# Kernel optimization log

Hardware: AMD Instinct MI355X
Metric: run time of the kernel (lower is better)

The kernel has to match this reference:

```python
import jax, jax.numpy as jnp
import numpy as np

# ---- Cl(3,0,1) projective geometric algebra tables (GATr basis ordering) ----
_BASIS = [(), (0,), (1,), (2,), (3,),
          (0, 1), (0, 2), (0, 3), (1, 2), (1, 3), (2, 3),
          (0, 1, 2), (0, 1, 3), (0, 2, 3), (1, 2, 3), (0, 1, 2, 3)]
_IDX = {b: i for i, b in enumerate(_BASIS)}
_METRIC = (0.0, 1.0, 1.0, 1.0)  # e0^2 = 0, e1^2 = e2^2 = e3^2 = 1


def _blade_product(a, b):
    arr = list(a) + list(b)
    sign = 1.0
    for i in range(len(arr)):
        for j in range(len(arr) - 1):
            if arr[j] > arr[j + 1]:
                arr[j], arr[j + 1] = arr[j + 1], arr[j]
                sign = -sign
    out, i = [], 0
    while i < len(arr):
        if i + 1 < len(arr) and arr[i] == arr[i + 1]:
            sign *= _METRIC[arr[i]]
            i += 2
        else:
            out.append(arr[i])
            i += 1
    return sign, tuple(out)


def _build_cayley():
    c = np.zeros((16, 16, 16), np.float32)
    for i, a in enumerate(_BASIS):
        for j, b in enumerate(_BASIS):
            s, blade = _blade_product(a, b)
            if s != 0.0:
                c[i, j, _IDX[blade]] += s
    return c

_CAYLEY = _build_cayley()                      # (16,16,16) geometric-product table
_DUAL_FLIP = np.arange(15, -1, -1)             # index reversal permutation
_DUAL_SIGNS = np.array([_blade_product(_BASIS[15 - j], _BASIS[j])[0] for j in range(16)], np.float32)


def _embed_point(p):
    # GATr-style PGA point embedding into trivector components: mv dim 16
    mv = jnp.zeros(p.shape[:-1] + (16,), p.dtype)
    mv = mv.at[..., 14].set(1.0)          # e123 (homogeneous coord)
    mv = mv.at[..., 13].set(p[..., 0])    # e023 <- x
    mv = mv.at[..., 12].set(-p[..., 1])   # e013 <- -y
    mv = mv.at[..., 11].set(p[..., 2])    # e012 <- z
    return mv


def _nn_gather(query, points):
    # brute-force K=1 NN: for each query point return its nearest neighbor in `points`
    # squared distances (B,N,M) via ||q||^2 + ||p||^2 - 2 q.p
    d = (jnp.sum(query * query, -1)[..., :, None]
         + jnp.sum(points * points, -1)[..., None, :]
         - 2.0 * jnp.einsum('bnd,bmd->bnm', query, points))
    idx = jnp.argmin(d, axis=-1)  # (B,N) int32
    return jnp.take_along_axis(points, idx[..., None], axis=1)  # (B,N,3)


def _geometric_product_loss(pred, tgt):
    cayley = jnp.asarray(_CAYLEY, pred.dtype)
    gp = jnp.einsum('ijk,...i,...j->...k', cayley, pred, tgt)  # (B,N,16)
    diff = pred - tgt
    dual = jnp.asarray(_DUAL_SIGNS, diff.dtype) * diff[..., _DUAL_FLIP]
    loss = jnp.mean(jnp.linalg.norm(gp, axis=-1) + jnp.linalg.norm(dual, axis=-1))
    # normalize to [0,1] with min_loss=1.0, max_loss=3.0
    return jnp.clip((loss - 1.0) / 2.0, 0.0, 1.0)


def setup_inputs() -> dict:
    key = jax.random.key(0)
    k1, k2 = jax.random.split(key)
    B, N = 2, 8192
    return {
        'source_points': jax.random.normal(k1, (B, N, 3), jnp.float32),
        'target_points': jax.random.normal(k2, (B, N, 3), jnp.float32),
    }


def reference(source_points, target_points):
    # source -> nearest target, target -> nearest source
    new_target_points = _nn_gather(source_points, target_points)  # (B,N,3)
    new_source_points = _nn_gather(target_points, source_points)  # (B,N,3)

    mv_source = _embed_point(source_points)
    mv_target = _embed_point(target_points)
    mv_new_source = _embed_point(new_source_points)
    mv_new_target = _embed_point(new_target_points)

    gp_loss_t2s = _geometric_product_loss(mv_source, mv_new_target)
    gp_loss_s2t = _geometric_product_loss(mv_new_source, mv_target)
    return 0.5 * (gp_loss_t2s + gp_loss_s2t)
```

## Files before the change

### kernel.cpp

```cpp
#include <hip/hip_runtime.h>


typedef short short8 __attribute__((ext_vector_type(8)));
typedef float f32x16 __attribute__((ext_vector_type(16)));

#define PPB      1024
#define PS       8
#define LDS_HALF 576
#define LDS_TILE 1152


__device__ __forceinline__ unsigned short bf16h(float f) {
    unsigned u = __float_as_uint(f);
    return (unsigned short)((u + 0x7fffu + ((u >> 16) & 1u)) >> 16);
}
__device__ __forceinline__ float bf16v(unsigned short h) {
    return __uint_as_float((unsigned)h << 16);
}

__global__ __launch_bounds__(256, 4)
void fused_kernel(const float* __restrict__ src, const float* __restrict__ tgt,
                  unsigned* __restrict__ chunkCnt, unsigned* __restrict__ finalCnt,
                  unsigned* __restrict__ accP, unsigned* __restrict__ d2min,
                  float* __restrict__ out, int N) {
    __shared__ __align__(16) unsigned char Alds[32 * LDS_TILE];

    const int t   = threadIdx.x;
    const int l   = t & 63, w = t >> 6;
    const int nqc = N >> 8;
    const int bpt = nqc * PS;
    const int task = blockIdx.x / bpt;
    const int rem  = blockIdx.x % bpt;
    const int qc = rem / PS, pc = rem % PS;

    const int pcloud = task ^ 2;
    const float* pRaw = (pcloud < 2 ? src : tgt)
                        + (size_t)3 * ((size_t)(pcloud & 1) * N + (size_t)pc * PPB);
    #pragma unroll
    for (int k = 0; k < 4; ++k) {
        const int j = t + k * 256;
        const float x = pRaw[3*j], y = pRaw[3*j+1], z = pRaw[3*j+2];
        const float pp = x*x + y*y + z*z;
        unsigned short A16[16];
        const float p3[3] = {x, y, z};
        #pragma unroll
        for (int d = 0; d < 3; ++d) {
            const float m2 = -2.0f * p3[d];
            const unsigned short th = bf16h(m2);
            A16[d] = th; A16[4+d] = th; A16[8+d] = bf16h(m2 - bf16v(th));
        }
        const unsigned short pph = bf16h(pp);
        A16[3] = pph; A16[7] = bf16h(pp - bf16v(pph)); A16[11] = 0;
        A16[12] = A16[13] = A16[14] = A16[15] = 0;
        const int tile = j >> 5, r = j & 31;
        unsigned char* base = Alds + tile * LDS_TILE + r * 16 + (r >> 3) * 16;
        *(short8*)(base)            = *(const short8*)(A16);
        *(short8*)(base + LDS_HALF) = *(const short8*)(A16 + 8);
    }

    const int col = l & 31, h = l >> 5;
    const float* qRaw = (task < 2 ? src : tgt)
                        + (size_t)3 * (size_t)((task & 1) * N);
    const int qloc = qc * 256 + w * 64 + col;
    float qa[3], qb[3];
    #pragma unroll
    for (int d = 0; d < 3; ++d) {
        qa[d] = qRaw[3*qloc + d];
        qb[d] = qRaw[3*(qloc+32) + d];
    }
    const float qqa = qa[0]*qa[0] + qa[1]*qa[1] + qa[2]*qa[2];
    const float qqb = qb[0]*qb[0] + qb[1]*qb[1] + qb[2]*qb[2];

    unsigned short B0[8], B1[8];
    #pragma unroll
    for (int d = 0; d < 3; ++d) {
        const unsigned short ha = bf16h(qa[d]);
        const unsigned short hb = bf16h(qb[d]);
        B0[d] = ha; B1[d] = hb;
        B0[4+d] = (h == 0) ? bf16h(qa[d] - bf16v(ha)) : (unsigned short)0;
        B1[4+d] = (h == 0) ? bf16h(qb[d] - bf16v(hb)) : (unsigned short)0;
    }
    B0[3] = B0[7] = (h == 0) ? (unsigned short)0x3F80 : (unsigned short)0;
    B1[3] = B1[7] = B0[3];
    const short8 b0 = *(const short8*)B0;
    const short8 b1 = *(const short8*)B1;

    __syncthreads();

    const int lbase = h * LDS_HALF + col * 16 + (col >> 3) * 16;
    float best0 = 3.4e38f, best1 = 3.4e38f;
    const f32x16 zero = {};
    #pragma unroll 4
    for (int i = 0; i < 32; ++i) {
        const short8 a = *(const short8*)(Alds + i * LDS_TILE + lbase);
        f32x16 d0 = __builtin_amdgcn_mfma_f32_32x32x16_bf16(a, b0, zero, 0, 0, 0);
        f32x16 d1 = __builtin_amdgcn_mfma_f32_32x32x16_bf16(a, b1, zero, 0, 0, 0);
        best0 = fminf(fminf(d0[0],  d0[1]),  best0);
        best0 = fminf(fminf(d0[2],  d0[3]),  best0);
        best0 = fminf(fminf(d0[4],  d0[5]),  best0);
        best0 = fminf(fminf(d0[6],  d0[7]),  best0);
        best0 = fminf(fminf(d0[8],  d0[9]),  best0);
        best0 = fminf(fminf(d0[10], d0[11]), best0);
        best0 = fminf(fminf(d0[12], d0[13]), best0);
        best0 = fminf(fminf(d0[14], d0[15]), best0);
        best1 = fminf(fminf(d1[0],  d1[1]),  best1);
        best1 = fminf(fminf(d1[2],  d1[3]),  best1);
        best1 = fminf(fminf(d1[4],  d1[5]),  best1);
        best1 = fminf(fminf(d1[6],  d1[7]),  best1);
        best1 = fminf(fminf(d1[8],  d1[9]),  best1);
        best1 = fminf(fminf(d1[10], d1[11]), best1);
        best1 = fminf(fminf(d1[12], d1[13]), best1);
        best1 = fminf(fminf(d1[14], d1[15]), best1);
    }

    best0 = fminf(best0, __shfl_xor(best0, 32));
    best1 = fminf(best1, __shfl_xor(best1, 32));
    const int qbase = task * N + qc * 256;
    if (l < 32) {
        const int q0 = qbase + w * 64 + l;
        unsigned o0 = atomicMin(&d2min[q0],
                                __float_as_uint(fmaxf(best0 + qqa, 0.0f)));
        unsigned o1 = atomicMin(&d2min[q0 + 32],
                                __float_as_uint(fmaxf(best1 + qqb, 0.0f)));
        asm volatile("" :: "v"(o0), "v"(o1));
    }

    __shared__ int lastChunk;
    __syncthreads();
    if (t == 0)
        lastChunk = (atomicAdd(&chunkCnt[task * nqc + qc], 1u)
                     == 0x7f7f7f7fu + (unsigned)PS - 1u);
    __syncthreads();
    if (!lastChunk) return;

    const float d2 = __uint_as_float(atomicOr(&d2min[qbase + t], 0u));
    double fv = (double)(sqrtf(1.0f + d2) + sqrtf(d2));
    #pragma unroll
    for (int o = 32; o > 0; o >>= 1) fv += __shfl_down(fv, o);
    __shared__ double wsum[4];
    __shared__ int lastFinal;
    if (l == 0) wsum[w] = fv;
    __syncthreads();
    if (t == 0) {
        const float csum = (float)(wsum[0] + wsum[1] + wsum[2] + wsum[3]);
        unsigned oldA = atomicExch(&accP[task * nqc + qc], __float_as_uint(csum));
        asm volatile("" :: "v"(oldA));
        lastFinal = (atomicAdd(finalCnt, 1u)
                     == 0x7f7f7f7fu + (unsigned)(4 * nqc) - 1u);
    }
    __syncthreads();
    if (!lastFinal) return;

    __shared__ float pvals[128];
    const int ncid = 4 * nqc;
    if (t < ncid) pvals[t] = __uint_as_float(atomicOr(&accP[t], 0u));
    __syncthreads();
    if (t == 0) {
        double s0 = 0.0, s1 = 0.0;
        for (int i = 0; i < ncid / 2; ++i)        s0 += (double)pvals[i];
        for (int i = ncid / 2; i < ncid; ++i)     s1 += (double)pvals[i];
        const double inv = 1.0 / (double)(2 * N);
        double l0 = (s0 * inv - 1.0) * 0.5;
        double l1 = (s1 * inv - 1.0) * 0.5;
        l0 = l0 < 0.0 ? 0.0 : (l0 > 1.0 ? 1.0 : l0);
        l1 = l1 < 0.0 ? 0.0 : (l1 > 1.0 ? 1.0 : l1);
        out[0] = (float)(0.5 * (l0 + l1));
    }
}

extern "C" void kernel_launch(void* const* d_in, const int* in_sizes, int n_in,
                              void* d_out, int out_size, void* d_ws, size_t ws_size,
                              hipStream_t stream) {
    const float* src = (const float*)d_in[0];
    const float* tgt = (const float*)d_in[1];
    float* out = (float*)d_out;

    const int twoN = in_sizes[0] / 3;
    const int N    = twoN / 2;
    const int QT   = 4 * N;

    unsigned* chunkCnt = (unsigned*)d_ws;
    unsigned* finalCnt = (unsigned*)((char*)d_ws + 512);
    unsigned* accP     = (unsigned*)((char*)d_ws + 1024);
    unsigned* d2min    = (unsigned*)((char*)d_ws + 2048);

    hipMemsetAsync(d_ws, 0x7f, 2048 + (size_t)QT * sizeof(unsigned), stream);

    const int blocks = 4 * (N >> 8) * PS;
    fused_kernel<<<blocks, 256, 0, stream>>>(src, tgt, chunkCnt, finalCnt,
                                             accP, d2min, out, N);
}
```

Baseline: 24.78 us.

## Give each block full point range with double-buffered LDS, drop atomicMin merge

The work split changes from query-chunk × point-chunk blocks (1024 blocks, 256 queries each) to 256 blocks of 128 queries that each scan all 8192 points. Point chunks are staged through a double-buffered LDS pair, so the next chunk is prepared while the current one is processed. This removes the global atomicMin buffer, the per-chunk counters and the large memset, and the final reduction becomes a shuffle-based double-precision sum. The trade-off is fewer blocks, which lowers parallelism and occupancy across the GPU's CUs, and each block now runs a much longer serial loop.

```diff
diff --git a/kernel.cpp b/kernel.cpp
--- a/kernel.cpp
+++ b/kernel.cpp
@@ -4,10 +4,10 @@
 typedef short short8 __attribute__((ext_vector_type(8)));
 typedef float f32x16 __attribute__((ext_vector_type(16)));
 
-#define PPB      1024
-#define PS       8
 #define LDS_HALF 576
 #define LDS_TILE 1152
+#define CHUNK    1024
+#define NCHUNK   8
 
 
 __device__ __forceinline__ unsigned short bf16h(float f) {
@@ -18,147 +18,151 @@
     return __uint_as_float((unsigned)h << 16);
 }
 
-__global__ __launch_bounds__(256, 4)
+__global__ __launch_bounds__(256)
 void fused_kernel(const float* __restrict__ src, const float* __restrict__ tgt,
-                  unsigned* __restrict__ chunkCnt, unsigned* __restrict__ finalCnt,
-                  unsigned* __restrict__ accP, unsigned* __restrict__ d2min,
+                  unsigned* __restrict__ finalCnt,
+                  unsigned long long* __restrict__ accP,
                   float* __restrict__ out, int N) {
-    __shared__ __align__(16) unsigned char Alds[32 * LDS_TILE];
+    __shared__ __align__(16) unsigned char Alds[2][32 * LDS_TILE];
 
     const int t   = threadIdx.x;
     const int l   = t & 63, w = t >> 6;
-    const int nqc = N >> 8;
-    const int bpt = nqc * PS;
-    const int task = blockIdx.x / bpt;
-    const int rem  = blockIdx.x % bpt;
-    const int qc = rem / PS, pc = rem % PS;
-
-    const int pcloud = task ^ 2;
-    const float* pRaw = (pcloud < 2 ? src : tgt)
-                        + (size_t)3 * ((size_t)(pcloud & 1) * N + (size_t)pc * PPB);
-    #pragma unroll
-    for (int k = 0; k < 4; ++k) {
-        const int j = t + k * 256;
-        const float x = pRaw[3*j], y = pRaw[3*j+1], z = pRaw[3*j+2];
-        const float pp = x*x + y*y + z*z;
-        unsigned short A16[16];
-        const float p3[3] = {x, y, z};
-        #pragma unroll
-        for (int d = 0; d < 3; ++d) {
-            const float m2 = -2.0f * p3[d];
-            const unsigned short th = bf16h(m2);
-            A16[d] = th; A16[4+d] = th; A16[8+d] = bf16h(m2 - bf16v(th));
-        }
-        const unsigned short pph = bf16h(pp);
-        A16[3] = pph; A16[7] = bf16h(pp - bf16v(pph)); A16[11] = 0;
-        A16[12] = A16[13] = A16[14] = A16[15] = 0;
-        const int tile = j >> 5, r = j & 31;
-        unsigned char* base = Alds + tile * LDS_TILE + r * 16 + (r >> 3) * 16;
-        *(short8*)(base)            = *(const short8*)(A16);
-        *(short8*)(base + LDS_HALF) = *(const short8*)(A16 + 8);
-    }
+    const int nqc = N >> 7;
+    const int task = blockIdx.x / nqc;
+    const int qc   = blockIdx.x % nqc;
 
     const int col = l & 31, h = l >> 5;
     const float* qRaw = (task < 2 ? src : tgt)
                         + (size_t)3 * (size_t)((task & 1) * N);
-    const int qloc = qc * 256 + w * 64 + col;
-    float qa[3], qb[3];
+    const int qloc = qc * 128 + w * 32 + col;
+    float q3[3];
+    #pragma unroll
+    for (int d = 0; d < 3; ++d) q3[d] = qRaw[3 * qloc + d];
+    const float qq = q3[0]*q3[0] + q3[1]*q3[1] + q3[2]*q3[2];
+
+    unsigned short B8[8];
     #pragma unroll
     for (int d = 0; d < 3; ++d) {
-        qa[d] = qRaw[3*qloc + d];
-        qb[d] = qRaw[3*(qloc+32) + d];
+        const unsigned short qh = bf16h(q3[d]);
+        B8[d] = qh;
+        B8[4 + d] = (h == 0) ? bf16h(q3[d] - bf16v(qh)) : (unsigned short)0;
     }
-    const float qqa = qa[0]*qa[0] + qa[1]*qa[1] + qa[2]*qa[2];
-    const float qqb = qb[0]*qb[0] + qb[1]*qb[1] + qb[2]*qb[2];
+    B8[3] = B8[7] = (h == 0) ? (unsigned short)0x3F80 : (unsigned short)0;
+    const short8 b = *(const short8*)B8;
 
-    unsigned short B0[8], B1[8];
-    #pragma unroll
-    for (int d = 0; d < 3; ++d) {
-        const unsigned short ha = bf16h(qa[d]);
-        const unsigned short hb = bf16h(qb[d]);
-        B0[d] = ha; B1[d] = hb;
-        B0[4+d] = (h == 0) ? bf16h(qa[d] - bf16v(ha)) : (unsigned short)0;
-        B1[4+d] = (h == 0) ? bf16h(qb[d] - bf16v(hb)) : (unsigned short)0;
+    const int pcloud = task ^ 2;
+    const float* pBase = (pcloud < 2 ? src : tgt)
+                         + (size_t)3 * (size_t)((pcloud & 1) * N);
+
+    {
+        const float* pRaw = pBase;
+        #pragma unroll
+        for (int k = 0; k < 4; ++k) {
+            const int j = t + k * 256;
+            const float x = pRaw[3*j], y = pRaw[3*j+1], z = pRaw[3*j+2];
+            const float pp = x*x + y*y + z*z;
+            unsigned short A16[16];
+            const float p3[3] = {x, y, z};
+            #pragma unroll
+            for (int d = 0; d < 3; ++d) {
+                const float m2 = -2.0f * p3[d];
+                const unsigned short th = bf16h(m2);
+                A16[d] = th; A16[4+d] = th; A16[8+d] = bf16h(m2 - bf16v(th));
+            }
+            const unsigned short pph = bf16h(pp);
+            A16[3] = pph; A16[7] = bf16h(pp - bf16v(pph)); A16[11] = 0;
+            A16[12] = A16[13] = A16[14] = A16[15] = 0;
+            const int tile = j >> 5, r = j & 31;
+            unsigned char* base = Alds[0] + tile * LDS_TILE + r * 16 + (r >> 3) * 16;
+            *(short8*)(base)            = *(const short8*)(A16);
+            *(short8*)(base + LDS_HALF) = *(const short8*)(A16 + 8);
+        }
     }
-    B0[3] = B0[7] = (h == 0) ? (unsigned short)0x3F80 : (unsigned short)0;
-    B1[3] = B1[7] = B0[3];
-    const short8 b0 = *(const short8*)B0;
-    const short8 b1 = *(const short8*)B1;
-
     __syncthreads();
 
     const int lbase = h * LDS_HALF + col * 16 + (col >> 3) * 16;
-    float best0 = 3.4e38f, best1 = 3.4e38f;
+    float best = 3.4e38f;
     const f32x16 zero = {};
-    #pragma unroll 4
-    for (int i = 0; i < 32; ++i) {
-        const short8 a = *(const short8*)(Alds + i * LDS_TILE + lbase);
-        f32x16 d0 = __builtin_amdgcn_mfma_f32_32x32x16_bf16(a, b0, zero, 0, 0, 0);
-        f32x16 d1 = __builtin_amdgcn_mfma_f32_32x32x16_bf16(a, b1, zero, 0, 0, 0);
-        best0 = fminf(fminf(d0[0],  d0[1]),  best0);
-        best0 = fminf(fminf(d0[2],  d0[3]),  best0);
-        best0 = fminf(fminf(d0[4],  d0[5]),  best0);
-        best0 = fminf(fminf(d0[6],  d0[7]),  best0);
-        best0 = fminf(fminf(d0[8],  d0[9]),  best0);
-        best0 = fminf(fminf(d0[10], d0[11]), best0);
-        best0 = fminf(fminf(d0[12], d0[13]), best0);
-        best0 = fminf(fminf(d0[14], d0[15]), best0);
-        best1 = fminf(fminf(d1[0],  d1[1]),  best1);
-        best1 = fminf(fminf(d1[2],  d1[3]),  best1);
-        best1 = fminf(fminf(d1[4],  d1[5]),  best1);
-        best1 = fminf(fminf(d1[6],  d1[7]),  best1);
-        best1 = fminf(fminf(d1[8],  d1[9]),  best1);
-        best1 = fminf(fminf(d1[10], d1[11]), best1);
-        best1 = fminf(fminf(d1[12], d1[13]), best1);
-        best1 = fminf(fminf(d1[14], d1[15]), best1);
+    for (int c = 0; c < NCHUNK; ++c) {
+        const unsigned char* buf = Alds[c & 1];
+        #pragma unroll 4
+        for (int i = 0; i < 32; ++i) {
+            const short8 a = *(const short8*)(buf + i * LDS_TILE + lbase);
+            f32x16 d0 = __builtin_amdgcn_mfma_f32_32x32x16_bf16(a, b, zero, 0, 0, 0);
+            best = fminf(fminf(d0[0],  d0[1]),  best);
+            best = fminf(fminf(d0[2],  d0[3]),  best);
+            best = fminf(fminf(d0[4],  d0[5]),  best);
+            best = fminf(fminf(d0[6],  d0[7]),  best);
+            best = fminf(fminf(d0[8],  d0[9]),  best);
+            best = fminf(fminf(d0[10], d0[11]), best);
+            best = fminf(fminf(d0[12], d0[13]), best);
+            best = fminf(fminf(d0[14], d0[15]), best);
+        }
+        if (c + 1 < NCHUNK) {
+            const float* pRaw = pBase + (size_t)3 * (size_t)(c + 1) * CHUNK;
+            unsigned char* nbuf = Alds[(c + 1) & 1];
+            #pragma unroll
+            for (int k = 0; k < 4; ++k) {
+                const int j = t + k * 256;
+                const float x = pRaw[3*j], y = pRaw[3*j+1], z = pRaw[3*j+2];
+                const float pp = x*x + y*y + z*z;
+                unsigned short A16[16];
+                const float p3[3] = {x, y, z};
+                #pragma unroll
+                for (int d = 0; d < 3; ++d) {
+                    const float m2 = -2.0f * p3[d];
+                    const unsigned short th = bf16h(m2);
+                    A16[d] = th; A16[4+d] = th; A16[8+d] = bf16h(m2 - bf16v(th));
+                }
+                const unsigned short pph = bf16h(pp);
+                A16[3] = pph; A16[7] = bf16h(pp - bf16v(pph)); A16[11] = 0;
+                A16[12] = A16[13] = A16[14] = A16[15] = 0;
+                const int tile = j >> 5, r = j & 31;
+                unsigned char* base = nbuf + tile * LDS_TILE + r * 16 + (r >> 3) * 16;
+                *(short8*)(base)            = *(const short8*)(A16);
+                *(short8*)(base + LDS_HALF) = *(const short8*)(A16 + 8);
+            }
+        }
+        __syncthreads();
     }
 
-    best0 = fminf(best0, __shfl_xor(best0, 32));
-    best1 = fminf(best1, __shfl_xor(best1, 32));
-    const int qbase = task * N + qc * 256;
+    best = fminf(best, __shfl_xor(best, 32));
+    double fv = 0.0;
     if (l < 32) {
-        const int q0 = qbase + w * 64 + l;
-        unsigned o0 = atomicMin(&d2min[q0],
-                                __float_as_uint(fmaxf(best0 + qqa, 0.0f)));
-        unsigned o1 = atomicMin(&d2min[q0 + 32],
-                                __float_as_uint(fmaxf(best1 + qqb, 0.0f)));
-        asm volatile("" :: "v"(o0), "v"(o1));
+        const float d2 = fmaxf(best + qq, 0.0f);
+        fv = (double)(sqrtf(1.0f + d2) + sqrtf(d2));
     }
-
-    __shared__ int lastChunk;
-    __syncthreads();
-    if (t == 0)
-        lastChunk = (atomicAdd(&chunkCnt[task * nqc + qc], 1u)
-                     == 0x7f7f7f7fu + (unsigned)PS - 1u);
-    __syncthreads();
-    if (!lastChunk) return;
-
-    const float d2 = __uint_as_float(atomicOr(&d2min[qbase + t], 0u));
-    double fv = (double)(sqrtf(1.0f + d2) + sqrtf(d2));
     #pragma unroll
     for (int o = 32; o > 0; o >>= 1) fv += __shfl_down(fv, o);
+
     __shared__ double wsum[4];
     __shared__ int lastFinal;
     if (l == 0) wsum[w] = fv;
     __syncthreads();
     if (t == 0) {
-        const float csum = (float)(wsum[0] + wsum[1] + wsum[2] + wsum[3]);
-        unsigned oldA = atomicExch(&accP[task * nqc + qc], __float_as_uint(csum));
-        asm volatile("" :: "v"(oldA));
-        lastFinal = (atomicAdd(finalCnt, 1u)
-                     == 0x7f7f7f7fu + (unsigned)(4 * nqc) - 1u);
+        const double bs = (wsum[0] + wsum[1]) + (wsum[2] + wsum[3]);
+        atomicExch(&accP[blockIdx.x], __double_as_longlong(bs));
+        asm volatile("s_waitcnt vmcnt(0)" ::: "memory");
+        lastFinal = (atomicAdd(finalCnt, 1u) == 0x7f7f7f7fu + 255u);
     }
     __syncthreads();
     if (!lastFinal) return;
 
-    __shared__ float pvals[128];
-    const int ncid = 4 * nqc;
-    if (t < ncid) pvals[t] = __uint_as_float(atomicOr(&accP[t], 0u));
+    const double pv = __longlong_as_double(
+        (long long)atomicOr(&accP[t], 0ull));
+    double a0 = (t < 128) ? pv : 0.0;
+    double a1 = (t < 128) ? 0.0 : pv;
+    #pragma unroll
+    for (int o = 32; o > 0; o >>= 1) {
+        a0 += __shfl_down(a0, o);
+        a1 += __shfl_down(a1, o);
+    }
+    __shared__ double fs0[4], fs1[4];
+    if (l == 0) { fs0[w] = a0; fs1[w] = a1; }
     __syncthreads();
     if (t == 0) {
-        double s0 = 0.0, s1 = 0.0;
-        for (int i = 0; i < ncid / 2; ++i)        s0 += (double)pvals[i];
-        for (int i = ncid / 2; i < ncid; ++i)     s1 += (double)pvals[i];
+        const double s0 = (fs0[0] + fs0[1]) + (fs0[2] + fs0[3]);
+        const double s1 = (fs1[0] + fs1[1]) + (fs1[2] + fs1[3]);
         const double inv = 1.0 / (double)(2 * N);
         double l0 = (s0 * inv - 1.0) * 0.5;
         double l1 = (s1 * inv - 1.0) * 0.5;
@@ -177,16 +181,12 @@
 
     const int twoN = in_sizes[0] / 3;
     const int N    = twoN / 2;
-    const int QT   = 4 * N;
 
-    unsigned* chunkCnt = (unsigned*)d_ws;
-    unsigned* finalCnt = (unsigned*)((char*)d_ws + 512);
-    unsigned* accP     = (unsigned*)((char*)d_ws + 1024);
-    unsigned* d2min    = (unsigned*)((char*)d_ws + 2048);
+    unsigned* finalCnt        = (unsigned*)d_ws;
+    unsigned long long* accP  = (unsigned long long*)((char*)d_ws + 1024);
 
-    hipMemsetAsync(d_ws, 0x7f, 2048 + (size_t)QT * sizeof(unsigned), stream);
+    hipMemsetAsync(d_ws, 0x7f, 512, stream);
 
-    const int blocks = 4 * (N >> 8) * PS;
-    fused_kernel<<<blocks, 256, 0, stream>>>(src, tgt, chunkCnt, finalCnt,
-                                             accP, d2min, out, N);
+    const int blocks = 4 * (N >> 7);
+    fused_kernel<<<blocks, 256, 0, stream>>>(src, tgt, finalCnt, accP, out, N);
 }
```

Measured after the change: 38.19 us. +54.1%, slower.
